# Optimization experiments

Hardware: AMD Instinct MI355X
Metric: run time of the kernel (lower is better)

Reference implementation:

```python
import jax, jax.numpy as jnp
import numpy as np

SIGMA = 0.4            # gaussian geodesic kernel width (class default)
B, N_IN, N_OUT, C, K = 2, 163842, 40962, 128, 7  # icosphere rank 7 -> rank 6, valence-7 candidates


def setup_inputs() -> dict:
    key = jax.random.key(0)
    k_x, k_p, k_o, k_c, k_d = jax.random.split(key, 5)
    x = jax.random.normal(k_x, (B, N_IN, C), dtype=jnp.float32)
    parent_idx = jax.random.randint(k_p, (N_IN,), 0, N_OUT)
    omega = jax.random.uniform(k_o, (N_IN,), dtype=jnp.float32, minval=0.5, maxval=1.5)
    omega = omega / omega.mean()          # matches omega / omega.mean() in __init__
    cand_idx = jax.random.randint(k_c, (N_IN, K), 0, N_OUT)
    cand_mask = jnp.ones((N_IN, K), dtype=jnp.float32)
    delta = jax.random.uniform(k_d, (N_IN, K), dtype=jnp.float32, minval=0.0, maxval=0.5)
    return dict(x=x, omega=omega, delta=delta, cand_mask=cand_mask,
                parent_idx=parent_idx, cand_idx=cand_idx)


def reference(x, omega, delta, cand_mask, parent_idx, cand_idx):
    # --- AreaWeightedDownsample: weight, scatter-add to coarse nodes, normalize ---
    weighted = x * omega[None, :, None]                        # [B, N_in, C]
    down = jnp.zeros((x.shape[0], N_OUT, x.shape[2]), x.dtype)
    down = down.at[:, parent_idx].add(weighted)                # scatter_add over node dim
    denom = jnp.zeros((N_OUT,), x.dtype).at[parent_idx].add(omega)
    down = down / jnp.clip(denom, 1e-8)[None, :, None]         # [B, N_out, C]
    # --- GeodesicKernelUpsample: gather K coarse candidates, gaussian geodesic weights ---
    w = jnp.exp(-(delta * delta) / (2.0 * SIGMA * SIGMA)) * cand_mask   # [N_in, K]
    w = w / jnp.clip(w.sum(axis=-1, keepdims=True), 1e-8)
    gathered = down[:, cand_idx]                               # [B, N_in, K, C]
    return jnp.einsum('nk,bnkc->bnc', w, gathered)             # [B, N_in, C]
```

## Files before the change

### kernel.cpp

```cpp
#include <hip/hip_runtime.h>
#include <hip/hip_bf16.h>

#define B_SZ   2
#define N_IN   163842
#define N_OUT  40962
#define C_DIM  128
#define K_CAND 7
#define INV_2SIG2 3.125f

typedef float f32x4 __attribute__((ext_vector_type(4)));
typedef unsigned short u16x8 __attribute__((ext_vector_type(8)));

__device__ __forceinline__ float bf2f(unsigned short u) {
    return __uint_as_float((unsigned)u << 16);
}
__device__ __forceinline__ unsigned short f2bf(float f) {
    unsigned u = __float_as_uint(f);
    return (unsigned short)((u + 0x7fffu + ((u >> 16) & 1u)) >> 16);
}

__global__ __launch_bounds__(256) void count_kernel(
    const int* __restrict__ parent, int* __restrict__ count)
{
    int n = blockIdx.x * 256 + threadIdx.x;
    if (n < N_IN) atomicAdd(&count[parent[n]], 1);
}

#define SCAN_T 1024
#define PER_T  41
__global__ __launch_bounds__(SCAN_T) void scan_kernel(
    const int* __restrict__ count, int* __restrict__ offs)
{
    __shared__ int sh[SCAN_T];
    const int t = threadIdx.x;
    const int base = t * PER_T;
    int local[PER_T];
    int sum = 0;
    #pragma unroll
    for (int i = 0; i < PER_T; ++i) {
        const int j = base + i;
        const int c = (j < N_OUT) ? count[j] : 0;
        local[i] = sum;
        sum += c;
    }
    sh[t] = sum;
    __syncthreads();
    for (int off = 1; off < SCAN_T; off <<= 1) {
        int v = (t >= off) ? sh[t - off] : 0;
        __syncthreads();
        sh[t] += v;
        __syncthreads();
    }
    const int ebase = sh[t] - sum;
    #pragma unroll
    for (int i = 0; i < PER_T; ++i) {
        const int j = base + i;
        if (j < N_OUT) offs[j] = ebase + local[i];
    }
}

__global__ __launch_bounds__(256) void fill_kernel(
    const int* __restrict__ parent, const int* __restrict__ offs,
    const float* __restrict__ omega,
    int* __restrict__ count, int* __restrict__ perm,
    float* __restrict__ om_perm)
{
    int n = blockIdx.x * 256 + threadIdx.x;
    if (n < N_IN) {
        const int p = parent[n];
        const float om = omega[n];
        const int pos = offs[p] + atomicSub(&count[p], 1) - 1;
        perm[pos] = n;
        om_perm[pos] = om;
    }
}

__global__ __launch_bounds__(256) void reduce_kernel(
    const float* __restrict__ x,
    const int*   __restrict__ offs,
    const int*   __restrict__ perm,
    const float* __restrict__ om_perm,
    __hip_bfloat16* __restrict__ down)
{
    const int wid  = threadIdx.x >> 6;
    const int lane = threadIdx.x & 63;
    const int p = blockIdx.x * 4 + wid;
    if (p >= N_OUT) return;

    const int beg = offs[p];
    const int end = (p + 1 < N_OUT) ? offs[p + 1] : N_IN;
    const int cnt = end - beg;

    const int half = lane >> 5;
    const int l    = lane & 31;
    const f32x4* x4 = (const f32x4*)x;
    const size_t bofs = (size_t)half * N_IN * 32;

    f32x4 acc = {0.f, 0.f, 0.f, 0.f};
    float ds = 0.f;

    for (int cbase = 0; cbase < cnt; cbase += 64) {
        const int m = min(64, cnt - cbase);
        int   myn  = 0;
        float myom = 0.f;
        if (lane < m) {
            myn  = perm[beg + cbase + lane];
            myom = om_perm[beg + cbase + lane];
        }
        for (int j = 0; j < m; ++j) {
            const int   n  = __shfl(myn,  j);
            const float om = __shfl(myom, j);
            ds += om;
            const f32x4 v = __builtin_nontemporal_load(&x4[bofs + (size_t)n * 32 + l]);
            acc.x = fmaf(v.x, om, acc.x);
            acc.y = fmaf(v.y, om, acc.y);
            acc.z = fmaf(v.z, om, acc.z);
            acc.w = fmaf(v.w, om, acc.w);
        }
    }
    const float inv = 1.f / fmaxf(ds, 1e-8f);

    ushort4 hh;
    hh.x = f2bf(acc.x * inv);
    hh.y = f2bf(acc.y * inv);
    hh.z = f2bf(acc.z * inv);
    hh.w = f2bf(acc.w * inv);
    ((ushort4*)down)[((size_t)half * N_OUT + p) * 32 + l] = hh;
}

__global__ __launch_bounds__(256) void gather_kernel(
    const float* __restrict__ delta,
    const float* __restrict__ cand_mask,
    const int*   __restrict__ cand_idx,
    const __hip_bfloat16* __restrict__ down,
    float* __restrict__ out)
{
    const int wid  = threadIdx.x >> 6;
    const int lane = threadIdx.x & 63;
    const int grp  = lane >> 5;
    const int l5   = lane & 31;
    const int n    = blockIdx.x * 8 + wid * 2 + grp;
    if (n >= N_IN) return;

    float w = 0.f;
    int pidx = 0;
    if (l5 < K_CAND) {
        const float d   = __builtin_nontemporal_load(&delta[(size_t)n * K_CAND + l5]);
        const float msk = __builtin_nontemporal_load(&cand_mask[(size_t)n * K_CAND + l5]);
        pidx = __builtin_nontemporal_load(&cand_idx[(size_t)n * K_CAND + l5]);
        w = __expf(-d * d * INV_2SIG2) * msk;
    }
    float s = w;
    s += __shfl_xor(s, 1, 8);
    s += __shfl_xor(s, 2, 8);
    s += __shfl_xor(s, 4, 8);
    const float coef = w / fmaxf(s, 1e-8f);

    float cf[K_CAND];
    int   pk[K_CAND];
    #pragma unroll
    for (int k = 0; k < K_CAND; ++k) {
        cf[k] = __shfl(coef, k, 32);
        pk[k] = __shfl(pidx, k, 32);
    }

    const int half = l5 >> 4;
    const int l4   = l5 & 15;
    const u16x8* d8 = (const u16x8*)down;
    const size_t bofs = (size_t)half * N_OUT * 16;

    u16x8 v[K_CAND];
    #pragma unroll
    for (int k = 0; k < K_CAND; ++k)
        v[k] = d8[bofs + (size_t)pk[k] * 16 + l4];

    f32x4 acc0 = {0.f, 0.f, 0.f, 0.f};
    f32x4 acc1 = {0.f, 0.f, 0.f, 0.f};
    #pragma unroll
    for (int k = 0; k < K_CAND; ++k) {
        const float c = cf[k];
        acc0.x = fmaf(c, bf2f(v[k].s0), acc0.x);
        acc0.y = fmaf(c, bf2f(v[k].s1), acc0.y);
        acc0.z = fmaf(c, bf2f(v[k].s2), acc0.z);
        acc0.w = fmaf(c, bf2f(v[k].s3), acc0.w);
        acc1.x = fmaf(c, bf2f(v[k].s4), acc1.x);
        acc1.y = fmaf(c, bf2f(v[k].s5), acc1.y);
        acc1.z = fmaf(c, bf2f(v[k].s6), acc1.z);
        acc1.w = fmaf(c, bf2f(v[k].s7), acc1.w);
    }
    f32x4* o4 = (f32x4*)out;
    const size_t obase = ((size_t)half * N_IN + n) * 32 + (size_t)l4 * 2;
    __builtin_nontemporal_store(acc0, &o4[obase]);
    __builtin_nontemporal_store(acc1, &o4[obase + 1]);
}

extern "C" void kernel_launch(void* const* d_in, const int* in_sizes, int n_in,
                              void* d_out, int out_size, void* d_ws, size_t ws_size,
                              hipStream_t stream) {
    const float* x         = (const float*)d_in[0];
    const float* omega     = (const float*)d_in[1];
    const float* delta     = (const float*)d_in[2];
    const float* cand_mask = (const float*)d_in[3];
    const int*   parent    = (const int*)d_in[4];
    const int*   cand_idx  = (const int*)d_in[5];
    float* out = (float*)d_out;

    __hip_bfloat16* down = (__hip_bfloat16*)d_ws;
    int*   count   = (int*)(down + (size_t)B_SZ * N_OUT * C_DIM);
    int*   offs    = count + N_OUT;
    int*   perm    = offs + N_OUT;
    float* om_perm = (float*)(perm + N_IN);

    hipMemsetAsync(count, 0, (size_t)N_OUT * sizeof(int), stream);

    const int nblk = (N_IN + 255) / 256;
    count_kernel<<<nblk, 256, 0, stream>>>(parent, count);
    scan_kernel<<<1, SCAN_T, 0, stream>>>(count, offs);
    fill_kernel<<<nblk, 256, 0, stream>>>(parent, offs, omega, count, perm, om_perm);
    reduce_kernel<<<(N_OUT + 3) / 4, 256, 0, stream>>>(x, offs, perm, om_perm, down);
    gather_kernel<<<(N_IN + 7) / 8, 256, 0, stream>>>(
        delta, cand_mask, cand_idx, down, out);
}
```

Before: 433.5 us.

## Parallelize scan across blocks, unroll reduce loop, process two rows per gather group

The single-block serial scan is replaced with a three-kernel multi-block scan built on wavefront shuffles, which removes a long single-CU serial phase. The reduce inner loop gets unroll 4 so more x loads can be in flight at once. The gather kernel now handles two output rows per 32-lane group, issuing 14 independent candidate loads per thread and halving the grid size. In exchange it adds two kernel launches, raises register pressure in gather, and drops the nontemporal hints on the delta, mask and index loads.

```diff
diff --git a/kernel.cpp b/kernel.cpp
--- a/kernel.cpp
+++ b/kernel.cpp
@@ -8,6 +8,9 @@
 #define K_CAND 7
 #define INV_2SIG2 3.125f
 
+#define SCAN_T 1024
+#define NBLK_SCAN ((N_OUT + SCAN_T - 1) / SCAN_T)
+
 typedef float f32x4 __attribute__((ext_vector_type(4)));
 typedef unsigned short u16x8 __attribute__((ext_vector_type(8)));
 
@@ -26,37 +29,58 @@
     if (n < N_IN) atomicAdd(&count[parent[n]], 1);
 }
 
-#define SCAN_T 1024
-#define PER_T  41
-__global__ __launch_bounds__(SCAN_T) void scan_kernel(
-    const int* __restrict__ count, int* __restrict__ offs)
-{
-    __shared__ int sh[SCAN_T];
-    const int t = threadIdx.x;
-    const int base = t * PER_T;
-    int local[PER_T];
-    int sum = 0;
-    #pragma unroll
-    for (int i = 0; i < PER_T; ++i) {
-        const int j = base + i;
-        const int c = (j < N_OUT) ? count[j] : 0;
-        local[i] = sum;
-        sum += c;
-    }
-    sh[t] = sum;
+__global__ __launch_bounds__(SCAN_T) void scan1_kernel(
+    const int* __restrict__ count, int* __restrict__ offs, int* __restrict__ bsum)
+{
+    __shared__ int wsum[SCAN_T / 64];
+    const int t    = threadIdx.x;
+    const int lane = t & 63;
+    const int wid  = t >> 6;
+    const int j    = blockIdx.x * SCAN_T + t;
+    const int c = (j < N_OUT) ? count[j] : 0;
+
+    int v = c;
+    #pragma unroll
+    for (int off = 1; off < 64; off <<= 1) {
+        int u = __shfl_up(v, off, 64);
+        if (lane >= off) v += u;
+    }
+    if (lane == 63) wsum[wid] = v;
     __syncthreads();
-    for (int off = 1; off < SCAN_T; off <<= 1) {
-        int v = (t >= off) ? sh[t - off] : 0;
-        __syncthreads();
-        sh[t] += v;
-        __syncthreads();
-    }
-    const int ebase = sh[t] - sum;
-    #pragma unroll
-    for (int i = 0; i < PER_T; ++i) {
-        const int j = base + i;
-        if (j < N_OUT) offs[j] = ebase + local[i];
-    }
+    if (wid == 0 && lane < SCAN_T / 64) {
+        int w = wsum[lane];
+        #pragma unroll
+        for (int off = 1; off < SCAN_T / 64; off <<= 1) {
+            int u = __shfl_up(w, off, 64);
+            if (lane >= off) w += u;
+        }
+        wsum[lane] = w;
+    }
+    __syncthreads();
+    const int wbase = (wid == 0) ? 0 : wsum[wid - 1];
+    if (j < N_OUT) offs[j] = wbase + v - c;
+    if (t == 0) bsum[blockIdx.x] = wsum[SCAN_T / 64 - 1];
+}
+
+__global__ __launch_bounds__(64) void scan2_kernel(
+    const int* __restrict__ bsum, int* __restrict__ bbase)
+{
+    const int lane = threadIdx.x;
+    int s = (lane < NBLK_SCAN) ? bsum[lane] : 0;
+    int v = s;
+    #pragma unroll
+    for (int off = 1; off < 64; off <<= 1) {
+        int u = __shfl_up(v, off, 64);
+        if (lane >= off) v += u;
+    }
+    if (lane < NBLK_SCAN) bbase[lane] = v - s;
+}
+
+__global__ __launch_bounds__(SCAN_T) void scan3_kernel(
+    int* __restrict__ offs, const int* __restrict__ bbase)
+{
+    const int j = blockIdx.x * SCAN_T + threadIdx.x;
+    if (j < N_OUT && blockIdx.x > 0) offs[j] += bbase[blockIdx.x];
 }
 
 __global__ __launch_bounds__(256) void fill_kernel(
@@ -107,6 +131,7 @@
             myn  = perm[beg + cbase + lane];
             myom = om_perm[beg + cbase + lane];
         }
+        #pragma unroll 4
         for (int j = 0; j < m; ++j) {
             const int   n  = __shfl(myn,  j);
             const float om = __shfl(myom, j);
@@ -139,15 +164,19 @@
     const int lane = threadIdx.x & 63;
     const int grp  = lane >> 5;
     const int l5   = lane & 31;
-    const int n    = blockIdx.x * 8 + wid * 2 + grp;
-    if (n >= N_IN) return;
-
+    const int n0   = blockIdx.x * 16 + wid * 4 + grp * 2;
+    if (n0 >= N_IN) return;
+    const bool r1ok = (n0 + 1 < N_IN);
+
+    const int sub = l5 >> 3;
+    const int ls  = l5 & 7;
     float w = 0.f;
     int pidx = 0;
-    if (l5 < K_CAND) {
-        const float d   = __builtin_nontemporal_load(&delta[(size_t)n * K_CAND + l5]);
-        const float msk = __builtin_nontemporal_load(&cand_mask[(size_t)n * K_CAND + l5]);
-        pidx = __builtin_nontemporal_load(&cand_idx[(size_t)n * K_CAND + l5]);
+    if (sub < 2 && ls < K_CAND && (sub == 0 || r1ok)) {
+        const int n = n0 + sub;
+        const float d   = delta[(size_t)n * K_CAND + ls];
+        const float msk = cand_mask[(size_t)n * K_CAND + ls];
+        pidx = cand_idx[(size_t)n * K_CAND + ls];
         w = __expf(-d * d * INV_2SIG2) * msk;
     }
     float s = w;
@@ -156,12 +185,15 @@
     s += __shfl_xor(s, 4, 8);
     const float coef = w / fmaxf(s, 1e-8f);
 
-    float cf[K_CAND];
-    int   pk[K_CAND];
-    #pragma unroll
-    for (int k = 0; k < K_CAND; ++k) {
-        cf[k] = __shfl(coef, k, 32);
-        pk[k] = __shfl(pidx, k, 32);
+    float cf[2][K_CAND];
+    int   pk[2][K_CAND];
+    #pragma unroll
+    for (int r = 0; r < 2; ++r) {
+        #pragma unroll
+        for (int k = 0; k < K_CAND; ++k) {
+            cf[r][k] = __shfl(coef, r * 8 + k, 32);
+            pk[r][k] = __shfl(pidx, r * 8 + k, 32);
+        }
     }
 
     const int half = l5 >> 4;
@@ -169,29 +201,36 @@
     const u16x8* d8 = (const u16x8*)down;
     const size_t bofs = (size_t)half * N_OUT * 16;
 
-    u16x8 v[K_CAND];
-    #pragma unroll
-    for (int k = 0; k < K_CAND; ++k)
-        v[k] = d8[bofs + (size_t)pk[k] * 16 + l4];
-
-    f32x4 acc0 = {0.f, 0.f, 0.f, 0.f};
-    f32x4 acc1 = {0.f, 0.f, 0.f, 0.f};
-    #pragma unroll
-    for (int k = 0; k < K_CAND; ++k) {
-        const float c = cf[k];
-        acc0.x = fmaf(c, bf2f(v[k].s0), acc0.x);
-        acc0.y = fmaf(c, bf2f(v[k].s1), acc0.y);
-        acc0.z = fmaf(c, bf2f(v[k].s2), acc0.z);
-        acc0.w = fmaf(c, bf2f(v[k].s3), acc0.w);
-        acc1.x = fmaf(c, bf2f(v[k].s4), acc1.x);
-        acc1.y = fmaf(c, bf2f(v[k].s5), acc1.y);
-        acc1.z = fmaf(c, bf2f(v[k].s6), acc1.z);
-        acc1.w = fmaf(c, bf2f(v[k].s7), acc1.w);
-    }
+    u16x8 v[2][K_CAND];
+    #pragma unroll
+    for (int r = 0; r < 2; ++r)
+        #pragma unroll
+        for (int k = 0; k < K_CAND; ++k)
+            v[r][k] = d8[bofs + (size_t)pk[r][k] * 16 + l4];
+
     f32x4* o4 = (f32x4*)out;
-    const size_t obase = ((size_t)half * N_IN + n) * 32 + (size_t)l4 * 2;
-    __builtin_nontemporal_store(acc0, &o4[obase]);
-    __builtin_nontemporal_store(acc1, &o4[obase + 1]);
+    #pragma unroll
+    for (int r = 0; r < 2; ++r) {
+        f32x4 acc0 = {0.f, 0.f, 0.f, 0.f};
+        f32x4 acc1 = {0.f, 0.f, 0.f, 0.f};
+        #pragma unroll
+        for (int k = 0; k < K_CAND; ++k) {
+            const float c = cf[r][k];
+            acc0.x = fmaf(c, bf2f(v[r][k].s0), acc0.x);
+            acc0.y = fmaf(c, bf2f(v[r][k].s1), acc0.y);
+            acc0.z = fmaf(c, bf2f(v[r][k].s2), acc0.z);
+            acc0.w = fmaf(c, bf2f(v[r][k].s3), acc0.w);
+            acc1.x = fmaf(c, bf2f(v[r][k].s4), acc1.x);
+            acc1.y = fmaf(c, bf2f(v[r][k].s5), acc1.y);
+            acc1.z = fmaf(c, bf2f(v[r][k].s6), acc1.z);
+            acc1.w = fmaf(c, bf2f(v[r][k].s7), acc1.w);
+        }
+        if (r == 0 || r1ok) {
+            const size_t obase = ((size_t)half * N_IN + n0 + r) * 32 + (size_t)l4 * 2;
+            __builtin_nontemporal_store(acc0, &o4[obase]);
+            __builtin_nontemporal_store(acc1, &o4[obase + 1]);
+        }
+    }
 }
 
 extern "C" void kernel_launch(void* const* d_in, const int* in_sizes, int n_in,
@@ -210,14 +249,18 @@
     int*   offs    = count + N_OUT;
     int*   perm    = offs + N_OUT;
     float* om_perm = (float*)(perm + N_IN);
+    int*   bsum    = (int*)(om_perm + N_IN);
+    int*   bbase   = bsum + NBLK_SCAN;
 
     hipMemsetAsync(count, 0, (size_t)N_OUT * sizeof(int), stream);
 
     const int nblk = (N_IN + 255) / 256;
     count_kernel<<<nblk, 256, 0, stream>>>(parent, count);
-    scan_kernel<<<1, SCAN_T, 0, stream>>>(count, offs);
+    scan1_kernel<<<NBLK_SCAN, SCAN_T, 0, stream>>>(count, offs, bsum);
+    scan2_kernel<<<1, 64, 0, stream>>>(bsum, bbase);
+    scan3_kernel<<<NBLK_SCAN, SCAN_T, 0, stream>>>(offs, bbase);
     fill_kernel<<<nblk, 256, 0, stream>>>(parent, offs, omega, count, perm, om_perm);
     reduce_kernel<<<(N_OUT + 3) / 4, 256, 0, stream>>>(x, offs, perm, om_perm, down);
-    gather_kernel<<<(N_IN + 7) / 8, 256, 0, stream>>>(
+    gather_kernel<<<(N_IN + 15) / 16, 256, 0, stream>>>(
         delta, cand_mask, cand_idx, down, out);
 }
```

After: 397.1 us. 1.09x faster.
